# Kernel optimization log

Measured on AMD Instinct MI355X. Metric: run time of the kernel, lower is better.

The kernel has to match this reference:

```python
import jax, jax.numpy as jnp
import numpy as np

EPS = 1e-5


def _layer_norm(x, w, b):
    mu = jnp.mean(x, axis=-1, keepdims=True)
    var = jnp.mean(jnp.square(x - mu), axis=-1, keepdims=True)
    return (x - mu) * jax.lax.rsqrt(var + EPS) * w + b


def setup_inputs() -> dict:
    key = jax.random.key(0)
    ks = jax.random.split(key, 6)
    B, S, N, CM, CZ, H = 1, 512, 512, 64, 128, 8
    return {
        "m_si": jax.random.normal(ks[0], (B, S, N, CM), jnp.float32),
        "z_ij": jax.random.normal(ks[1], (B, S, S, CZ), jnp.float32),
        "ln_m_w": jnp.ones((CM,), jnp.float32),
        "ln_m_b": jnp.zeros((CM,), jnp.float32),
        "ln_z_w": jnp.ones((CZ,), jnp.float32),
        "ln_z_b": jnp.zeros((CZ,), jnp.float32),
        "W_v": jax.random.normal(ks[2], (CM, CM), jnp.float32) / np.sqrt(CM),
        "W_b": jax.random.normal(ks[3], (H, CZ), jnp.float32) / np.sqrt(CZ),
        "W_g": jax.random.normal(ks[4], (CM, CM), jnp.float32) / np.sqrt(CM),
        "W_out": jax.random.normal(ks[5], (CM, CM), jnp.float32) / np.sqrt(CM),
    }


def reference(m_si, z_ij, ln_m_w, ln_m_b, ln_z_w, ln_z_b, W_v, W_b, W_g, W_out):
    H = W_b.shape[0]
    *lead, S, N, CM = m_si.shape
    D = CM // H  # head_dim

    m = _layer_norm(m_si, ln_m_w, ln_m_b)  # (..., s, n, c_m)

    # Pair bias logits -> softmax over j (second sequence axis)
    b = _layer_norm(z_ij, ln_z_w, ln_z_b) @ W_b.T          # (..., i, j, h)
    w = jax.nn.softmax(b, axis=-2)                          # softmax over j

    v = (m @ W_v.T).reshape(*lead, S, N, H, D)              # (..., j, n, h, d)
    g = jax.nn.sigmoid(m @ W_g.T).reshape(*lead, S, N, H, D)

    o = jnp.einsum("...ijh,...jnhd->...inhd", w, v)         # pair-weighted avg
    out = (g * o).reshape(*lead, S, N, CM) @ W_out.T
    return out
```

## Files before the change

kernel.cpp:

```cpp
#include <hip/hip_runtime.h>

typedef __bf16 bf16x8 __attribute__((ext_vector_type(8)));
typedef float  f32x4  __attribute__((ext_vector_type(4)));
typedef unsigned short u16x8 __attribute__((ext_vector_type(8)));

__device__ __forceinline__ float b2f(unsigned short u) {
    unsigned int x = ((unsigned int)u) << 16;
    float f; __builtin_memcpy(&f, &x, 4); return f;
}
__device__ __forceinline__ unsigned short f2b(float f) {
    unsigned int x; __builtin_memcpy(&x, &f, 4);
    unsigned int r = (x + 0x7FFFu + ((x >> 16) & 1u)) >> 16;
    return (unsigned short)r;
}
__device__ __forceinline__ void async16(void* lds, const void* g) {
    __builtin_amdgcn_global_load_lds((const __attribute__((address_space(1))) void*)g,
                                     (__attribute__((address_space(3))) void*)lds, 16, 0, 0);
}

__global__ __launch_bounds__(256) void k0_wcvt(
    const float* __restrict__ Wv, const float* __restrict__ Wg, unsigned short* __restrict__ Wp)
{
    const int idx = blockIdx.x * 256 + threadIdx.x;
    const int cg = idx >> 10, col = (idx >> 3) & 127, u = idx & 7;
    const int k = cg * 8 + u;
    const float v = (col < 64) ? Wv[col * 64 + k] : Wg[(col - 64) * 64 + k];
    Wp[idx] = f2b(v);
}

__global__ __launch_bounds__(256) void k1_ln_vg(
    const float* __restrict__ m, const float* __restrict__ lnw, const float* __restrict__ lnb,
    const unsigned short* __restrict__ Wp,
    unsigned short* __restrict__ vT, unsigned short* __restrict__ gB)
{
    __shared__ __align__(16) unsigned short Wl[8192];
    __shared__ __align__(16) unsigned short mhb[2048];
    __shared__ float vstage[32][65];
    __shared__ float gstage[32][65];
    const int t = threadIdx.x, w = t >> 6, lane = t & 63;
    const int n = blockIdx.x, s0 = blockIdx.y * 32;

#pragma unroll
    for (int r = 0; r < 4; r++)
        async16(&Wl[(r * 256 + t) * 8], Wp + (size_t)(r * 256 + t) * 8);

    const int rl = t >> 3, cg = t & 7, c8 = cg * 8;
    {
        const int s = s0 + rl;
        const float* src = &m[((size_t)s * 512 + n) * 64 + c8];
        float4 x0 = *(const float4*)src;
        float4 x1 = *(const float4*)(src + 4);
        float sum = x0.x+x0.y+x0.z+x0.w + x1.x+x1.y+x1.z+x1.w;
        float sq  = x0.x*x0.x+x0.y*x0.y+x0.z*x0.z+x0.w*x0.w
                  + x1.x*x1.x+x1.y*x1.y+x1.z*x1.z+x1.w*x1.w;
#pragma unroll
        for (int msk = 4; msk; msk >>= 1) { sum += __shfl_xor(sum, msk); sq += __shfl_xor(sq, msk); }
        float mu  = sum * (1.f / 64.f);
        float var = sq * (1.f / 64.f) - mu * mu;
        float rs  = rsqrtf(var + 1e-5f);
        float4 lw0 = *(const float4*)&lnw[c8], lw1 = *(const float4*)&lnw[c8 + 4];
        float4 lb0 = *(const float4*)&lnb[c8], lb1 = *(const float4*)&lnb[c8 + 4];
        u16x8 hb;
        hb[0] = f2b((x0.x - mu) * rs * lw0.x + lb0.x);
        hb[1] = f2b((x0.y - mu) * rs * lw0.y + lb0.y);
        hb[2] = f2b((x0.z - mu) * rs * lw0.z + lb0.z);
        hb[3] = f2b((x0.w - mu) * rs * lw0.w + lb0.w);
        hb[4] = f2b((x1.x - mu) * rs * lw1.x + lb1.x);
        hb[5] = f2b((x1.y - mu) * rs * lw1.y + lb1.y);
        hb[6] = f2b((x1.z - mu) * rs * lw1.z + lb1.z);
        hb[7] = f2b((x1.w - mu) * rs * lw1.w + lb1.w);
        *(u16x8*)&mhb[(cg * 32 + rl) * 8] = hb;
    }
    __syncthreads();

    const int quad = lane >> 4, lq = lane & 15;
    const int colbase = w * 32;
    f32x4 zero = {0.f, 0.f, 0.f, 0.f};
    f32x4 acc[2][2] = {{zero, zero}, {zero, zero}};
    bf16x8 af[2][2], bfr[2][2];
#pragma unroll
    for (int kk = 0; kk < 2; kk++) {
        const int ch = kk * 4 + quad;
#pragma unroll
        for (int mi = 0; mi < 2; mi++)
            af[mi][kk] = *(const bf16x8*)&mhb[(ch * 32 + mi * 16 + lq) * 8];
#pragma unroll
        for (int ni = 0; ni < 2; ni++)
            bfr[ni][kk] = *(const bf16x8*)&Wl[(ch * 128 + colbase + ni * 16 + lq) * 8];
    }
#pragma unroll
    for (int mi = 0; mi < 2; mi++)
#pragma unroll
        for (int ni = 0; ni < 2; ni++)
#pragma unroll
            for (int kk = 0; kk < 2; kk++)
                acc[mi][ni] = __builtin_amdgcn_mfma_f32_16x16x32_bf16(af[mi][kk], bfr[ni][kk], acc[mi][ni], 0, 0, 0);

    if (w < 2) {
#pragma unroll
        for (int mi = 0; mi < 2; mi++)
#pragma unroll
            for (int ni = 0; ni < 2; ni++)
#pragma unroll
                for (int rr = 0; rr < 4; rr++)
                    vstage[mi * 16 + quad * 4 + rr][colbase + ni * 16 + lq] = acc[mi][ni][rr];
    } else {
#pragma unroll
        for (int mi = 0; mi < 2; mi++)
#pragma unroll
            for (int ni = 0; ni < 2; ni++)
#pragma unroll
                for (int rr = 0; rr < 4; rr++) {
                    float gg = 1.f / (1.f + __expf(-acc[mi][ni][rr]));
                    gstage[mi * 16 + quad * 4 + rr][colbase - 64 + ni * 16 + lq] = gg;
                }
    }
    __syncthreads();

    {
        const int h = t >> 5, d = (t >> 2) & 7, jc = t & 3;
        u16x8 pk;
#pragma unroll
        for (int u = 0; u < 8; u++) pk[u] = f2b(vstage[jc * 8 + u][h * 8 + d]);
        size_t off = (size_t)h * 2097152 + (size_t)(n * 8 + d) * 512 + (size_t)(s0 + jc * 8);
        *(u16x8*)(vT + off) = pk;
    }
    {
        u16x8 gk;
#pragma unroll
        for (int u = 0; u < 8; u++) gk[u] = f2b(gstage[rl][c8 + u]);
        *(u16x8*)(gB + ((size_t)(s0 + rl) * 512 + n) * 64 + c8) = gk;
    }
}

__global__ __launch_bounds__(256) void k2_ln_b(
    const float* __restrict__ z, const float* __restrict__ lnw, const float* __restrict__ lnb,
    const float* __restrict__ Wb, float* __restrict__ bL)
{
    __shared__ float zrow[4][132];
    const int t = threadIdx.x, w = t >> 6, lane = t & 63;
    const int h = lane & 7, cg = lane >> 3;
    float wb[16];
#pragma unroll
    for (int q = 0; q < 4; q++) {
        float4 a = *(const float4*)&Wb[h * 128 + cg * 16 + q * 4];
        wb[4*q+0]=a.x; wb[4*q+1]=a.y; wb[4*q+2]=a.z; wb[4*q+3]=a.w;
    }
    const float lw0 = lnw[lane], lw1 = lnw[64 + lane];
    const float lb0 = lnb[lane], lb1 = lnb[64 + lane];
    const int nw = gridDim.x * 4;
    for (int row = blockIdx.x * 4 + w; row < 262144; row += nw) {
        float x0 = z[(size_t)row * 128 + lane];
        float x1 = z[(size_t)row * 128 + 64 + lane];
        float sum = x0 + x1, sq = x0 * x0 + x1 * x1;
#pragma unroll
        for (int msk = 32; msk; msk >>= 1) { sum += __shfl_xor(sum, msk); sq += __shfl_xor(sq, msk); }
        float mu = sum * (1.f / 128.f);
        float var = sq * (1.f / 128.f) - mu * mu;
        float rs = rsqrtf(var + 1e-5f);
        zrow[w][lane]      = (x0 - mu) * rs * lw0 + lb0;
        zrow[w][64 + lane] = (x1 - mu) * rs * lw1 + lb1;
        float acc = 0.f;
#pragma unroll
        for (int q = 0; q < 4; q++) {
            float4 zz = *(float4*)&zrow[w][cg * 16 + q * 4];
            acc += zz.x*wb[4*q] + zz.y*wb[4*q+1] + zz.z*wb[4*q+2] + zz.w*wb[4*q+3];
        }
#pragma unroll
        for (int msk = 8; msk < 64; msk <<= 1) acc += __shfl_xor(acc, msk);
        if (lane < 8) bL[(size_t)row * 8 + lane] = acc;
    }
}

__global__ __launch_bounds__(256) void k3_softmax(
    const float* __restrict__ bL, unsigned short* __restrict__ wp)
{
    __shared__ float bl[8][520];
    const int t = threadIdx.x;
    const int i = blockIdx.x;
    const float* src = bL + (size_t)i * 4096;
#pragma unroll
    for (int q = 0; q < 4; q++) {
        float4 a = *(const float4*)&src[q * 1024 + t * 4];
        int idx = q * 1024 + t * 4;
        bl[(idx+0)&7][(idx+0)>>3] = a.x;
        bl[(idx+1)&7][(idx+1)>>3] = a.y;
        bl[(idx+2)&7][(idx+2)>>3] = a.z;
        bl[(idx+3)&7][(idx+3)>>3] = a.w;
    }
    __syncthreads();
    const int h = t >> 5, l32 = t & 31;
    float vals[16];
    float mx = -1e30f;
#pragma unroll
    for (int jj = 0; jj < 16; jj++) { vals[jj] = bl[h][l32 + 32 * jj]; mx = fmaxf(mx, vals[jj]); }
#pragma unroll
    for (int msk = 1; msk < 32; msk <<= 1) mx = fmaxf(mx, __shfl_xor(mx, msk, 32));
    float s = 0.f;
#pragma unroll
    for (int jj = 0; jj < 16; jj++) { vals[jj] = __expf(vals[jj] - mx); s += vals[jj]; }
#pragma unroll
    for (int msk = 1; msk < 32; msk <<= 1) s += __shfl_xor(s, msk, 32);
    const float inv = 1.f / s;
    unsigned short* dst = wp + (size_t)h * 262144 + (size_t)i * 512;
#pragma unroll
    for (int jj = 0; jj < 16; jj++) dst[l32 + 32 * jj] = f2b(vals[jj] * inv);
}

__global__ __launch_bounds__(256) void k4_einsum(
    const unsigned short* __restrict__ wp, const unsigned short* __restrict__ vT,
    const unsigned short* __restrict__ gB, unsigned short* __restrict__ go)
{
    __shared__ __align__(16) unsigned short As[128 * 32];
    __shared__ __align__(16) unsigned short Bs[128 * 32];
    const int t = threadIdx.x;
    const int c0 = blockIdx.x * 128, i0 = blockIdx.y * 128, h = blockIdx.z;
    const unsigned short* Ab = wp + (size_t)h * 262144;
    const unsigned short* Bb = vT + (size_t)h * 2097152;
    const int w = t >> 6, lane = t & 63, quad = lane >> 4, lq = lane & 15;
    const int wi = w >> 1, wc = w & 1;

    f32x4 zero = {0.f, 0.f, 0.f, 0.f};
    f32x4 acc[4][4];
#pragma unroll
    for (int mi = 0; mi < 4; mi++)
#pragma unroll
        for (int ni = 0; ni < 4; ni++) acc[mi][ni] = zero;

    for (int k0 = 0; k0 < 512; k0 += 32) {
#pragma unroll
        for (int r = 0; r < 2; r++) {
            int idx = r * 256 + t;
            int row = idx >> 2, q = idx & 3;
            async16(&As[idx * 8], Ab + (size_t)(i0 + row) * 512 + k0 + q * 8);
            async16(&Bs[idx * 8], Bb + (size_t)(c0 + row) * 512 + k0 + q * 8);
        }
        __syncthreads();
        bf16x8 af[4], bfr[4];
#pragma unroll
        for (int mi = 0; mi < 4; mi++)
            af[mi] = *(const bf16x8*)&As[(wi * 64 + mi * 16 + lq) * 32 + quad * 8];
#pragma unroll
        for (int ni = 0; ni < 4; ni++)
            bfr[ni] = *(const bf16x8*)&Bs[(wc * 64 + ni * 16 + lq) * 32 + quad * 8];
#pragma unroll
        for (int mi = 0; mi < 4; mi++)
#pragma unroll
            for (int ni = 0; ni < 4; ni++)
                acc[mi][ni] = __builtin_amdgcn_mfma_f32_16x16x32_bf16(af[mi], bfr[ni], acc[mi][ni], 0, 0, 0);
        __syncthreads();
    }
#pragma unroll
    for (int mi = 0; mi < 4; mi++)
#pragma unroll
        for (int ni = 0; ni < 4; ni++)
#pragma unroll
            for (int rr = 0; rr < 4; rr++) {
                int ii = i0 + wi * 64 + mi * 16 + quad * 4 + rr;
                int c  = c0 + wc * 64 + ni * 16 + lq;
                size_t off = ((size_t)ii * 512 + (c >> 3)) * 64 + h * 8 + (c & 7);
                float gv = b2f(gB[off]);
                go[off] = f2b(acc[mi][ni][rr] * gv);
            }
}

__global__ __launch_bounds__(256) void k5_out(
    const unsigned short* __restrict__ go, const float* __restrict__ Wo, float* __restrict__ out)
{
    __shared__ float grow[4][64];
    const int t = threadIdx.x, w = t >> 6, lane = t & 63;
    float wo[64];
#pragma unroll
    for (int q = 0; q < 16; q++) {
        float4 a = *(const float4*)&Wo[lane * 64 + q * 4];
        wo[4*q+0]=a.x; wo[4*q+1]=a.y; wo[4*q+2]=a.z; wo[4*q+3]=a.w;
    }
    const int nw = gridDim.x * 4;
    for (int row = blockIdx.x * 4 + w; row < 262144; row += nw) {
        grow[w][lane] = b2f(go[(size_t)row * 64 + lane]);
        float acc = 0.f;
#pragma unroll
        for (int q = 0; q < 16; q++) {
            float4 gg = *(float4*)&grow[w][q * 4];
            acc += gg.x*wo[4*q] + gg.y*wo[4*q+1] + gg.z*wo[4*q+2] + gg.w*wo[4*q+3];
        }
        out[(size_t)row * 64 + lane] = acc;
    }
}

extern "C" void kernel_launch(void* const* d_in, const int* in_sizes, int n_in,
                              void* d_out, int out_size, void* d_ws, size_t ws_size,
                              hipStream_t stream)
{
    (void)in_sizes; (void)n_in; (void)out_size; (void)ws_size;
    const float* m    = (const float*)d_in[0];
    const float* z    = (const float*)d_in[1];
    const float* lnmw = (const float*)d_in[2];
    const float* lnmb = (const float*)d_in[3];
    const float* lnzw = (const float*)d_in[4];
    const float* lnzb = (const float*)d_in[5];
    const float* Wv   = (const float*)d_in[6];
    const float* Wb   = (const float*)d_in[7];
    const float* Wg   = (const float*)d_in[8];
    const float* Wo   = (const float*)d_in[9];
    float* out = (float*)d_out;
    char* ws = (char*)d_ws;

    unsigned short* vT = (unsigned short*)(ws);
    unsigned short* wp = (unsigned short*)(ws + 33554432);
    unsigned short* gB = (unsigned short*)(ws + 37748736);
    float*          bL = (float*)(ws + 71303168);
    unsigned short* go = (unsigned short*)(ws + 79691776);
    unsigned short* Wp = wp;

    k0_wcvt   <<<dim3(32),      256, 0, stream>>>(Wv, Wg, Wp);
    k1_ln_vg  <<<dim3(512, 16), 256, 0, stream>>>(m, lnmw, lnmb, Wp, vT, gB);
    k2_ln_b   <<<dim3(1024),    256, 0, stream>>>(z, lnzw, lnzb, Wb, bL);
    k3_softmax<<<dim3(512),     256, 0, stream>>>(bL, wp);
    k4_einsum <<<dim3(32, 4, 8),256, 0, stream>>>(wp, vT, gB, go);
    k5_out    <<<dim3(2048),    256, 0, stream>>>(go, Wo, out);
}
```

Baseline: 447.9 us.

## Use MFMA for output projection and 4-thread-per-row pair-bias LayerNorm

The output projection kernel becomes a bf16 MFMA GEMM. W_out is split into hi and lo bf16 parts staged in LDS to keep close to fp32 accuracy, replacing per-row scalar dot products that went through shared memory. The pair-bias LayerNorm kernel now gives four threads to each row, using float4 loads with W_b and the LN params held in LDS. This drops the wave-wide shuffles and the loop over rows. Both changes target instruction-bound scalar loops, and the trade-off is extra weight conversion per block plus new launch geometry.

```diff
diff --git a/kernel.cpp b/kernel.cpp
--- a/kernel.cpp
+++ b/kernel.cpp
@@ -137,39 +137,57 @@
     const float* __restrict__ z, const float* __restrict__ lnw, const float* __restrict__ lnb,
     const float* __restrict__ Wb, float* __restrict__ bL)
 {
-    __shared__ float zrow[4][132];
-    const int t = threadIdx.x, w = t >> 6, lane = t & 63;
-    const int h = lane & 7, cg = lane >> 3;
-    float wb[16];
-#pragma unroll
-    for (int q = 0; q < 4; q++) {
-        float4 a = *(const float4*)&Wb[h * 128 + cg * 16 + q * 4];
-        wb[4*q+0]=a.x; wb[4*q+1]=a.y; wb[4*q+2]=a.z; wb[4*q+3]=a.w;
-    }
-    const float lw0 = lnw[lane], lw1 = lnw[64 + lane];
-    const float lb0 = lnb[lane], lb1 = lnb[64 + lane];
-    const int nw = gridDim.x * 4;
-    for (int row = blockIdx.x * 4 + w; row < 262144; row += nw) {
-        float x0 = z[(size_t)row * 128 + lane];
-        float x1 = z[(size_t)row * 128 + 64 + lane];
-        float sum = x0 + x1, sq = x0 * x0 + x1 * x1;
-#pragma unroll
-        for (int msk = 32; msk; msk >>= 1) { sum += __shfl_xor(sum, msk); sq += __shfl_xor(sq, msk); }
-        float mu = sum * (1.f / 128.f);
-        float var = sq * (1.f / 128.f) - mu * mu;
-        float rs = rsqrtf(var + 1e-5f);
-        zrow[w][lane]      = (x0 - mu) * rs * lw0 + lb0;
-        zrow[w][64 + lane] = (x1 - mu) * rs * lw1 + lb1;
-        float acc = 0.f;
-#pragma unroll
-        for (int q = 0; q < 4; q++) {
-            float4 zz = *(float4*)&zrow[w][cg * 16 + q * 4];
-            acc += zz.x*wb[4*q] + zz.y*wb[4*q+1] + zz.z*wb[4*q+2] + zz.w*wb[4*q+3];
+    __shared__ float swb[1024];
+    __shared__ float sw[128], sb[128];
+    const int t = threadIdx.x;
+    const int gtid = blockIdx.x * 256 + t;
+    const int row = gtid >> 2, qt = gtid & 3;
+
+    const float* src = z + (size_t)row * 128;
+    float4 x[8];
+#pragma unroll
+    for (int q = 0; q < 8; q++)
+        x[q] = *(const float4*)&src[q * 16 + qt * 4];
+
+    *(float4*)&swb[t * 4] = *(const float4*)&Wb[t * 4];
+    if (t < 32)      *(float4*)&sw[t * 4] = *(const float4*)&lnw[t * 4];
+    else if (t < 64) *(float4*)&sb[(t - 32) * 4] = *(const float4*)&lnb[(t - 32) * 4];
+    __syncthreads();
+
+    float sum = 0.f, sq = 0.f;
+#pragma unroll
+    for (int q = 0; q < 8; q++) {
+        sum += x[q].x + x[q].y + x[q].z + x[q].w;
+        sq  += x[q].x*x[q].x + x[q].y*x[q].y + x[q].z*x[q].z + x[q].w*x[q].w;
+    }
+    sum += __shfl_xor(sum, 1); sq += __shfl_xor(sq, 1);
+    sum += __shfl_xor(sum, 2); sq += __shfl_xor(sq, 2);
+    const float mu  = sum * (1.f / 128.f);
+    const float var = sq * (1.f / 128.f) - mu * mu;
+    const float rs  = rsqrtf(var + 1e-5f);
+
+    float acc[8];
+#pragma unroll
+    for (int h = 0; h < 8; h++) acc[h] = 0.f;
+#pragma unroll
+    for (int q = 0; q < 8; q++) {
+        const int c0 = q * 16 + qt * 4;
+        const float4 lw = *(const float4*)&sw[c0];
+        const float4 lb = *(const float4*)&sb[c0];
+        const float zn0 = (x[q].x - mu) * rs * lw.x + lb.x;
+        const float zn1 = (x[q].y - mu) * rs * lw.y + lb.y;
+        const float zn2 = (x[q].z - mu) * rs * lw.z + lb.z;
+        const float zn3 = (x[q].w - mu) * rs * lw.w + lb.w;
+#pragma unroll
+        for (int h = 0; h < 8; h++) {
+            const float4 wv = *(const float4*)&swb[h * 128 + c0];
+            acc[h] += zn0 * wv.x + zn1 * wv.y + zn2 * wv.z + zn3 * wv.w;
         }
-#pragma unroll
-        for (int msk = 8; msk < 64; msk <<= 1) acc += __shfl_xor(acc, msk);
-        if (lane < 8) bL[(size_t)row * 8 + lane] = acc;
-    }
+    }
+#pragma unroll
+    for (int h = 0; h < 8; h++) { acc[h] += __shfl_xor(acc[h], 1); acc[h] += __shfl_xor(acc[h], 2); }
+    float2 o; o.x = acc[qt * 2]; o.y = acc[qt * 2 + 1];
+    *(float2*)&bL[(size_t)row * 8 + qt * 2] = o;
 }
 
 __global__ __launch_bounds__(256) void k3_softmax(
@@ -267,24 +285,48 @@
 __global__ __launch_bounds__(256) void k5_out(
     const unsigned short* __restrict__ go, const float* __restrict__ Wo, float* __restrict__ out)
 {
-    __shared__ float grow[4][64];
+    __shared__ __align__(16) unsigned short Bs[8192];
     const int t = threadIdx.x, w = t >> 6, lane = t & 63;
-    float wo[64];
-#pragma unroll
-    for (int q = 0; q < 16; q++) {
-        float4 a = *(const float4*)&Wo[lane * 64 + q * 4];
-        wo[4*q+0]=a.x; wo[4*q+1]=a.y; wo[4*q+2]=a.z; wo[4*q+3]=a.w;
-    }
-    const int nw = gridDim.x * 4;
-    for (int row = blockIdx.x * 4 + w; row < 262144; row += nw) {
-        grow[w][lane] = b2f(go[(size_t)row * 64 + lane]);
-        float acc = 0.f;
-#pragma unroll
-        for (int q = 0; q < 16; q++) {
-            float4 gg = *(float4*)&grow[w][q * 4];
-            acc += gg.x*wo[4*q] + gg.y*wo[4*q+1] + gg.z*wo[4*q+2] + gg.w*wo[4*q+3];
+    const int quad = lane >> 4, lq = lane & 15;
+
+    const int r0 = blockIdx.x * 64 + w * 16;
+    const unsigned short* Ab = go + (size_t)r0 * 64;
+    bf16x8 a[2];
+#pragma unroll
+    for (int kk = 0; kk < 2; kk++)
+        a[kk] = *(const bf16x8*)&Ab[lq * 64 + (kk * 4 + quad) * 8];
+
+#pragma unroll
+    for (int r = 0; r < 2; r++) {
+        const int idx = r * 256 + t;
+        const int ch = idx >> 6, col = idx & 63;
+        const float* srcw = &Wo[col * 64 + ch * 8];
+        float4 w0 = *(const float4*)srcw;
+        float4 w1 = *(const float4*)(srcw + 4);
+        float v[8] = {w0.x, w0.y, w0.z, w0.w, w1.x, w1.y, w1.z, w1.w};
+        u16x8 hi, lo;
+#pragma unroll
+        for (int u = 0; u < 8; u++) { hi[u] = f2b(v[u]); lo[u] = f2b(v[u] - b2f(hi[u])); }
+        *(u16x8*)&Bs[(ch * 64 + col) * 8] = hi;
+        *(u16x8*)&Bs[4096 + (ch * 64 + col) * 8] = lo;
+    }
+    __syncthreads();
+
+    f32x4 zero = {0.f, 0.f, 0.f, 0.f};
+#pragma unroll
+    for (int ni = 0; ni < 4; ni++) {
+        f32x4 acc = zero;
+#pragma unroll
+        for (int kk = 0; kk < 2; kk++) {
+            const int ko = (kk * 4 + quad) * 64;
+            bf16x8 bh = *(const bf16x8*)&Bs[(ko + ni * 16 + lq) * 8];
+            bf16x8 bl = *(const bf16x8*)&Bs[4096 + (ko + ni * 16 + lq) * 8];
+            acc = __builtin_amdgcn_mfma_f32_16x16x32_bf16(a[kk], bh, acc, 0, 0, 0);
+            acc = __builtin_amdgcn_mfma_f32_16x16x32_bf16(a[kk], bl, acc, 0, 0, 0);
         }
-        out[(size_t)row * 64 + lane] = acc;
+#pragma unroll
+        for (int rr = 0; rr < 4; rr++)
+            out[(size_t)(r0 + quad * 4 + rr) * 64 + ni * 16 + lq] = acc[rr];
     }
 }
 
@@ -315,8 +357,8 @@
 
     k0_wcvt   <<<dim3(32),      256, 0, stream>>>(Wv, Wg, Wp);
     k1_ln_vg  <<<dim3(512, 16), 256, 0, stream>>>(m, lnmw, lnmb, Wp, vT, gB);
-    k2_ln_b   <<<dim3(1024),    256, 0, stream>>>(z, lnzw, lnzb, Wb, bL);
+    k2_ln_b   <<<dim3(4096),    256, 0, stream>>>(z, lnzw, lnzb, Wb, bL);
     k3_softmax<<<dim3(512),     256, 0, stream>>>(bL, wp);
     k4_einsum <<<dim3(32, 4, 8),256, 0, stream>>>(wp, vT, gB, go);
-    k5_out    <<<dim3(2048),    256, 0, stream>>>(go, Wo, out);
-}
+    k5_out    <<<dim3(4096),    256, 0, stream>>>(go, Wo, out);
+}
```

Measured after the change: 369.0 us. -17.6%, faster.
